# Performance work log

Hardware: AMD Instinct MI355X
Metric: run time of the kernel (lower is better)

Reference implementation:

```python
import jax, jax.numpy as jnp
import numpy as np

N, P, H, K = 8192, 32, 512, 100
D = 2 * P
R = 32  # min(32, max(8, H))


def setup_inputs() -> dict:
    key = jax.random.key(0)
    ks = jax.random.split(key, 12)
    # strictly increasing event times
    dts = jax.random.uniform(ks[0], (N,), dtype=jnp.float32) * 0.1 + 1e-3
    times = jnp.cumsum(dts)
    marks = jax.random.randint(ks[1], (N,), 0, K, dtype=jnp.int32)
    u_inputs = jax.random.normal(ks[2], (N, H), dtype=jnp.float32) * 0.1
    # parameters (match torch init scales)
    lambda_log_real = jax.random.normal(ks[3], (P,), dtype=jnp.float32) * 0.1
    lambda_im = jax.random.normal(ks[4], (P,), dtype=jnp.float32) * 0.05
    V = jnp.eye(D, dtype=jnp.float32) + 0.01 * jax.random.normal(ks[5], (D, D), dtype=jnp.float32)
    B = jax.random.normal(ks[6], (D, H), dtype=jnp.float32) * 0.05
    E = jax.random.normal(ks[7], (D, R), dtype=jnp.float32) * 0.05
    alpha = jax.random.normal(ks[8], (R, K), dtype=jnp.float32) * 0.05
    gate_w = jax.random.normal(ks[9], (P, H), dtype=jnp.float32) * 0.02
    gate_b = jax.random.normal(ks[10], (P,), dtype=jnp.float32) * 0.02
    x0 = jnp.zeros((D,), dtype=jnp.float32)
    return {"times": times, "marks": marks, "u_inputs": u_inputs,
            "lambda_log_real": lambda_log_real, "lambda_im": lambda_im,
            "V": V, "B": B, "E": E, "alpha": alpha,
            "gate_w": gate_w, "gate_b": gate_b, "x0": x0}


def _v_block(V, pr, pi):
    """V @ blockdiag_p([[pr,-pi],[pi,pr]]) for each step n. V:(D,D), pr/pi:(n,P) -> (n,D,D)."""
    Dd = V.shape[0]
    Pp = pr.shape[-1]
    Vr = V.reshape(Dd, Pp, 2)
    col0 = Vr[None, :, :, 0] * pr[:, None, :] + Vr[None, :, :, 1] * pi[:, None, :]
    col1 = -Vr[None, :, :, 0] * pi[:, None, :] + Vr[None, :, :, 1] * pr[:, None, :]
    return jnp.stack([col0, col1], axis=-1).reshape(-1, Dd, Dd)


def reference(times, marks, u_inputs, lambda_log_real, lambda_im, V, B, E, alpha, gate_w, gate_b, x0):
    n = times.shape[0]
    dt = jnp.concatenate([times[:1], jnp.diff(times)])  # (N,) t_0 - 0, t_i - t_{i-1}
    # input-dependent eigenvalues: real = -softplus(log_real) * softplus(Wu+b), imag fixed
    gate = jax.nn.softplus(u_inputs @ gate_w.T + gate_b)           # (N,P)
    real = -jax.nn.softplus(lambda_log_real)[None, :] * gate        # (N,P)
    imag = jnp.broadcast_to(lambda_im[None, :], real.shape)         # (N,P)
    dtc = dt[:, None]
    exps = jnp.exp(real * dtc)
    cosb = jnp.cos(imag * dtc)
    sinb = jnp.sin(imag * dtc)
    a = exps * cosb  # Re(exp(lam dt))
    c = exps * sinb  # Im(exp(lam dt))
    V_inv = jnp.linalg.inv(V)
    # exp(A dt) = V M V^{-1}, M block-rotation per mode
    Aexp = _v_block(V, a, c) @ V_inv                                # (N,D,D)
    # integral (exp(lam dt) - 1)/lam, with dt fallback near lam=0
    denom = real * real + imag * imag
    num_re = a - 1.0
    num_im = c
    qr = (num_re * real + num_im * imag) / (denom + 1e-12)
    qi = (num_im * real - num_re * imag) / (denom + 1e-12)
    small = denom < 1e-8
    qr = jnp.where(small, dtc, qr)
    qi = jnp.where(small, 0.0, qi)
    VMint = _v_block(V, qr, qi)                                     # (N,D,D)
    # cont = V M_int V^{-1} B u  (fuse V^{-1} B u first, avoiding Kmat materialization)
    w = u_inputs @ (V_inv @ B).T                                    # (N,D)
    cont = jnp.einsum('nij,nj->ni', VMint, w)
    cont = jnp.where(dtc > 0, cont, 0.0)
    # mark impulses r_k = E alpha[:, k]
    r = (E @ alpha)[:, marks].T                                     # (N,D)

    def step(x_prev, inp):
        A_i, c_i, r_i = inp
        x_left = A_i @ x_prev + c_i
        x_right = x_left + r_i
        return x_right, (x_right, x_left)

    _, (x_right, x_left) = jax.lax.scan(step, x0, (Aexp, cont, r))
    return x_right, x_left
```

## Files before the change

### kernel.cpp

```cpp
#include <hip/hip_runtime.h>
#include <math.h>

#define NN 8192
#define PP 32
#define HH 512
#define KK 100
#define DD 64
#define RR 32
#define MM 96
#define CH 8
#define GG 1024

#define OFF_VINV   0
#define OFF_M      (OFF_VINV + DD*DD)
#define OFF_EAT    (OFF_M + MM*HH)
#define OFF_RHT    (OFF_EAT + KK*DD)
#define OFF_Y0     (OFF_RHT + KK*DD)
#define OFF_AGG    (OFF_Y0 + DD)
#define OFF_YST    (OFF_AGG + GG*PP*4)
#define OFF_C      (OFF_YST + GG*PP*2)

__device__ __forceinline__ float softplusf(float x) {
    return x > 20.f ? x : log1pf(expf(x));
}

#define IDX(r,c) ((r)*64 + ((c) ^ (((r)&7)<<2)))
__global__ __launch_bounds__(256) void kinv(const float* __restrict__ V,
                                            const float* __restrict__ x0,
                                            float* __restrict__ ws) {
    __shared__ float sm[16384];
    float* Vt = sm;
    float* X  = sm + 4096;
    float* Xt = sm + 8192;
    float* T  = sm + 12288;
    const int t  = threadIdx.x;
    const int i0 = (t >> 4) << 2;
    const int j0 = (t & 15) << 2;

    float nx[4][4];
    #pragma unroll
    for (int r = 0; r < 4; r++) {
        float4 v4 = *(const float4*)&V[(i0 + r) * DD + j0];
        float vv[4] = {v4.x, v4.y, v4.z, v4.w};
        #pragma unroll
        for (int s = 0; s < 4; s++) {
            Vt[IDX(j0 + s, i0 + r)] = vv[s];
            float xv = ((i0 + r) == (j0 + s) ? 2.f : 0.f) - vv[s];
            nx[r][s] = xv;
            X[IDX(i0 + r, j0 + s)] = xv;
            Xt[IDX(j0 + s, i0 + r)] = xv;
        }
    }
    __syncthreads();

    for (int it = 0; it < 3; it++) {
        float acc[4][4];
        #pragma unroll
        for (int r = 0; r < 4; r++)
            #pragma unroll
            for (int s = 0; s < 4; s++) acc[r][s] = 0.f;
        for (int k = 0; k < DD; k++) {
            float4 a = *(float4*)&Vt[IDX(k, i0)];
            float4 bb = *(float4*)&X[IDX(k, j0)];
            float av[4] = {a.x, a.y, a.z, a.w};
            float bv[4] = {bb.x, bb.y, bb.z, bb.w};
            #pragma unroll
            for (int r = 0; r < 4; r++)
                #pragma unroll
                for (int s = 0; s < 4; s++) acc[r][s] = fmaf(av[r], bv[s], acc[r][s]);
        }
        #pragma unroll
        for (int r = 0; r < 4; r++)
            *(float4*)&T[IDX(i0 + r, j0)] = make_float4(acc[r][0], acc[r][1], acc[r][2], acc[r][3]);
        __syncthreads();
        #pragma unroll
        for (int r = 0; r < 4; r++)
            #pragma unroll
            for (int s = 0; s < 4; s++) acc[r][s] = 0.f;
        for (int k = 0; k < DD; k++) {
            float4 a = *(float4*)&Xt[IDX(k, i0)];
            float4 bb = *(float4*)&T[IDX(k, j0)];
            float av[4] = {a.x, a.y, a.z, a.w};
            float bv[4] = {bb.x, bb.y, bb.z, bb.w};
            #pragma unroll
            for (int r = 0; r < 4; r++)
                #pragma unroll
                for (int s = 0; s < 4; s++) acc[r][s] = fmaf(av[r], bv[s], acc[r][s]);
        }
        #pragma unroll
        for (int r = 0; r < 4; r++) {
            float4 xo = *(float4*)&X[IDX(i0 + r, j0)];
            nx[r][0] = 2.f * xo.x - acc[r][0];
            nx[r][1] = 2.f * xo.y - acc[r][1];
            nx[r][2] = 2.f * xo.z - acc[r][2];
            nx[r][3] = 2.f * xo.w - acc[r][3];
        }
        __syncthreads();
        #pragma unroll
        for (int r = 0; r < 4; r++) {
            *(float4*)&X[IDX(i0 + r, j0)] = make_float4(nx[r][0], nx[r][1], nx[r][2], nx[r][3]);
            #pragma unroll
            for (int s = 0; s < 4; s++) Xt[IDX(j0 + s, i0 + r)] = nx[r][s];
        }
        __syncthreads();
    }
    #pragma unroll
    for (int r = 0; r < 4; r++)
        *(float4*)&ws[OFF_VINV + (i0 + r) * DD + j0] =
            make_float4(nx[r][0], nx[r][1], nx[r][2], nx[r][3]);
    float xw[4];
    #pragma unroll
    for (int s = 0; s < 4; s++) xw[s] = x0[j0 + s];
    #pragma unroll
    for (int r = 0; r < 4; r++) {
        float pr = nx[r][0] * xw[0] + nx[r][1] * xw[1] + nx[r][2] * xw[2] + nx[r][3] * xw[3];
        T[(i0 + r) * 17 + (t & 15)] = pr;
    }
    __syncthreads();
    if (t < DD) {
        float s = 0.f;
        #pragma unroll
        for (int jt = 0; jt < 16; jt++) s += T[t * 17 + jt];
        ws[OFF_Y0 + t] = s;
    }
}

__global__ __launch_bounds__(256) void kpre(const float* __restrict__ B,
                                            const float* __restrict__ E,
                                            const float* __restrict__ alpha,
                                            const float* __restrict__ gate_w,
                                            float* __restrict__ ws) {
    int b = blockIdx.x, t = threadIdx.x;
    if (b < 32) {
        int d = b * 2 + (t >> 7);
        int h0 = (t & 127) * 4;
        const float* vr = ws + OFF_VINV + d * DD;
        float4 acc = {0.f, 0.f, 0.f, 0.f};
        for (int j = 0; j < DD; j++) {
            float v = vr[j];
            float4 b4 = *(const float4*)&B[j * HH + h0];
            acc.x = fmaf(v, b4.x, acc.x); acc.y = fmaf(v, b4.y, acc.y);
            acc.z = fmaf(v, b4.z, acc.z); acc.w = fmaf(v, b4.w, acc.w);
        }
        *(float4*)&ws[OFF_M + (32 + d) * HH + h0] = acc;
    } else if (b < 34) {
        #pragma unroll
        for (int s = 0; s < 8; s++) {
            int i4 = (b - 32) * 2048 + t + 256 * s;
            ((float4*)(ws + OFF_M))[i4] = ((const float4*)gate_w)[i4];
        }
    } else {
        __shared__ float vi[DD * 65];
        __shared__ float ea_s[4][DD];
        int kk = (b - 34) * 4 + (t >> 6);
        int d = t & 63;
        for (int idx = t; idx < DD * DD; idx += 256)
            vi[(idx >> 6) * 65 + (idx & 63)] = ws[OFF_VINV + idx];
        float ea = 0.f;
        #pragma unroll
        for (int r = 0; r < RR; r++) ea = fmaf(E[d * RR + r], alpha[r * KK + kk], ea);
        ws[OFF_EAT + kk * DD + d] = ea;
        ea_s[t >> 6][d] = ea;
        __syncthreads();
        float rr = 0.f;
        for (int j = 0; j < DD; j++) rr = fmaf(vi[d * 65 + j], ea_s[t >> 6][j], rr);
        ws[OFF_RHT + kk * DD + d] = rr;
    }
}

__global__ __launch_bounds__(256) void kgemm(const float* __restrict__ u,
                                             float* __restrict__ ws) {
    __shared__ float uT[32 * 64];
    __shared__ float mT[96 * 64];
    int t = threadIdx.x;
    int n0 = blockIdx.x * 32;
    int tn = t & 15, tm = t >> 4;
    const float* Mg = ws + OFF_M;
    float acc[2][6];
    #pragma unroll
    for (int i = 0; i < 2; i++)
        #pragma unroll
        for (int j = 0; j < 6; j++) acc[i][j] = 0.f;

    for (int kc = 0; kc < HH; kc += 64) {
        #pragma unroll
        for (int s = 0; s < 2; s++) {
            int idx = t + 256 * s;
            int r = idx >> 4, c4 = idx & 15;
            float4 f4 = *(const float4*)&u[(n0 + r) * HH + kc + c4 * 4];
            *(float4*)&uT[r * 64 + ((c4 ^ ((r >> 2) & 7)) << 2)] = f4;
        }
        #pragma unroll
        for (int s = 0; s < 6; s++) {
            int idx = t + 256 * s;
            int r = idx >> 4, c4 = idx & 15;
            float4 f4 = *(const float4*)&Mg[r * HH + kc + c4 * 4];
            *(float4*)&mT[r * 64 + ((c4 ^ (r & 7)) << 2)] = f4;
        }
        __syncthreads();
        #pragma unroll
        for (int k4 = 0; k4 < 16; k4++) {
            float4 uu[2], mm[6];
            int swu = (tn >> 1) & 7;
            #pragma unroll
            for (int i = 0; i < 2; i++)
                uu[i] = *(float4*)&uT[(2 * tn + i) * 64 + ((k4 ^ swu) << 2)];
            #pragma unroll
            for (int j = 0; j < 6; j++) {
                int m = 6 * tm + j;
                mm[j] = *(float4*)&mT[m * 64 + ((k4 ^ (m & 7)) << 2)];
            }
            #pragma unroll
            for (int i = 0; i < 2; i++)
                #pragma unroll
                for (int j = 0; j < 6; j++)
                    acc[i][j] += uu[i].x * mm[j].x + uu[i].y * mm[j].y +
                                 uu[i].z * mm[j].z + uu[i].w * mm[j].w;
        }
        __syncthreads();
    }
    #pragma unroll
    for (int i = 0; i < 2; i++)
        #pragma unroll
        for (int j = 0; j < 6; j++)
            ws[OFF_C + (n0 + 2 * tn + i) * MM + 6 * tm + j] = acc[i][j];
}

__device__ __forceinline__ void coef_np(const float* __restrict__ ws,
                                        const int* __restrict__ marks,
                                        int n, int p, float dtv,
                                        float nlr, float imag, float gb,
                                        float& a, float& c, float& br, float& bi) {
    float gate = softplusf(ws[OFF_C + n * MM + p] + gb);
    float real = nlr * gate;
    float e = expf(real * dtv);
    a = e * cosf(imag * dtv);
    c = e * sinf(imag * dtv);
    float denom = real * real + imag * imag;
    float dn = denom + 1e-12f;
    float nre = a - 1.f, nim = c;
    float qr = (nre * real + nim * imag) / dn;
    float qi = (nim * real - nre * imag) / dn;
    if (denom < 1e-8f) { qr = dtv; qi = 0.f; }
    float2 w = *(const float2*)&ws[OFF_C + n * MM + 32 + 2 * p];
    br = qr * w.x - qi * w.y;
    bi = qr * w.y + qi * w.x;
    if (!(dtv > 0.f)) { br = 0.f; bi = 0.f; }
    int mk = marks[n];
    br += ws[OFF_RHT + mk * DD + 2 * p];
    bi += ws[OFF_RHT + mk * DD + 2 * p + 1];
}

__global__ __launch_bounds__(256) void kagg(const float* __restrict__ times,
                                            const int* __restrict__ marks,
                                            const float* __restrict__ llr,
                                            const float* __restrict__ lim,
                                            const float* __restrict__ gate_b,
                                            float* __restrict__ ws) {
    int b = blockIdx.x, t = threadIdx.x;
    int c = t >> 5, p = t & 31;
    int g = b * 8 + c, n0 = g * CH;
    float nlr = -softplusf(llr[p]);
    float imag = lim[p];
    float gb = gate_b[p];
    float zr = 1.f, zi = 0.f, Br = 0.f, Bi = 0.f;
    float tprev = (n0 == 0) ? 0.f : times[n0 - 1];
    for (int i = 0; i < CH; i++) {
        int n = n0 + i;
        float tcur = times[n];
        float dtv = tcur - tprev;
        tprev = tcur;
        float a, cc, br, bi;
        coef_np(ws, marks, n, p, dtv, nlr, imag, gb, a, cc, br, bi);
        float nzr = a * zr - cc * zi;
        float nzi = a * zi + cc * zr;
        float nBr = a * Br - cc * Bi + br;
        float nBi = a * Bi + cc * Br + bi;
        zr = nzr; zi = nzi; Br = nBr; Bi = nBi;
    }
    *(float4*)&ws[OFF_AGG + g * 128 + p * 4] = make_float4(zr, zi, Br, Bi);
}

__device__ __forceinline__ float4 comp_aff(float4 f, float4 g) {
    float4 r;
    r.x = f.x * g.x - f.y * g.y;
    r.y = f.x * g.y + f.y * g.x;
    r.z = f.x * g.z - f.y * g.w + f.z;
    r.w = f.x * g.w + f.y * g.z + f.w;
    return r;
}
__global__ __launch_bounds__(256) void kscan(float* __restrict__ ws) {
    __shared__ float4 sc[256];
    int p = blockIdx.x, t = threadIdx.x;
    float4 ag[4];
    #pragma unroll
    for (int j = 0; j < 4; j++)
        ag[j] = *(float4*)&ws[OFF_AGG + (4 * t + j) * 128 + p * 4];
    float4 val = ag[0];
    val = comp_aff(ag[1], val);
    val = comp_aff(ag[2], val);
    val = comp_aff(ag[3], val);
    sc[t] = val;
    __syncthreads();
    for (int s = 1; s < 256; s <<= 1) {
        float4 o = (t >= s) ? sc[t - s] : make_float4(1.f, 0.f, 0.f, 0.f);
        __syncthreads();
        if (t >= s) val = comp_aff(val, o);
        sc[t] = val;
        __syncthreads();
    }
    float4 Eb = (t > 0) ? sc[t - 1] : make_float4(1.f, 0.f, 0.f, 0.f);
    float2 y0v = *(float2*)&ws[OFF_Y0 + 2 * p];
    float2 ys;
    ys.x = Eb.x * y0v.x - Eb.y * y0v.y + Eb.z;
    ys.y = Eb.x * y0v.y + Eb.y * y0v.x + Eb.w;
    #pragma unroll
    for (int j = 0; j < 4; j++) {
        int g = 4 * t + j;
        *(float2*)&ws[OFF_YST + (g * 32 + p) * 2] = ys;
        float nyr = ag[j].x * ys.x - ag[j].y * ys.y + ag[j].z;
        float nyi = ag[j].x * ys.y + ag[j].y * ys.x + ag[j].w;
        ys.x = nyr; ys.y = nyi;
    }
}

__global__ __launch_bounds__(256) void kout(const float* __restrict__ V,
                                            const float* __restrict__ times,
                                            const int* __restrict__ marks,
                                            const float* __restrict__ llr,
                                            const float* __restrict__ lim,
                                            const float* __restrict__ gate_b,
                                            const float* __restrict__ ws,
                                            float* __restrict__ out) {
    __shared__ float vt[DD * 68];
    __shared__ float yl[DD * 68];
    int b = blockIdx.x, t = threadIdx.x;
    #pragma unroll
    for (int s = 0; s < 16; s++) {
        int idx = t + 256 * s;
        vt[(idx & 63) * 68 + (idx >> 6)] = V[idx];
    }
    int c = t >> 5, p = t & 31;
    int g = b * 8 + c, n0g = g * CH;
    int nb = b * 64;
    float2 y = *(const float2*)&ws[OFF_YST + (g * 32 + p) * 2];
    float nlr = -softplusf(llr[p]);
    float imag = lim[p];
    float gb = gate_b[p];
    float tprev = (n0g == 0) ? 0.f : times[n0g - 1];
    for (int i = 0; i < CH; i++) {
        int n = n0g + i;
        float tcur = times[n];
        float dtv = tcur - tprev;
        tprev = tcur;
        float a, cc, br, bi;
        coef_np(ws, marks, n, p, dtv, nlr, imag, gb, a, cc, br, bi);
        float nyr = a * y.x - cc * y.y + br;
        float nyi = a * y.y + cc * y.x + bi;
        y.x = nyr; y.y = nyi;
        int nl = c * 8 + i;
        *(float2*)&yl[nl * 68 + 2 * p] = y;
    }
    __syncthreads();
    int dt4 = (t & 15) * 4, nt4 = (t >> 4) * 4;
    float acc[4][4];
    #pragma unroll
    for (int r = 0; r < 4; r++)
        #pragma unroll
        for (int s = 0; s < 4; s++) acc[r][s] = 0.f;
    for (int k = 0; k < DD; k++) {
        float4 vv = *(float4*)&vt[k * 68 + dt4];
        float va[4] = {vv.x, vv.y, vv.z, vv.w};
        float yv[4];
        #pragma unroll
        for (int r = 0; r < 4; r++) yv[r] = yl[(nt4 + r) * 68 + k];
        #pragma unroll
        for (int r = 0; r < 4; r++)
            #pragma unroll
            for (int s = 0; s < 4; s++) acc[r][s] = fmaf(yv[r], va[s], acc[r][s]);
    }
    #pragma unroll
    for (int r = 0; r < 4; r++) {
        int n = nb + nt4 + r;
        int mk = marks[n];
        float4 o4 = make_float4(acc[r][0], acc[r][1], acc[r][2], acc[r][3]);
        *(float4*)&out[n * DD + dt4] = o4;
        float4 e4 = *(const float4*)&ws[OFF_EAT + mk * DD + dt4];
        o4.x -= e4.x; o4.y -= e4.y; o4.z -= e4.z; o4.w -= e4.w;
        *(float4*)&out[NN * DD + n * DD + dt4] = o4;
    }
}

extern "C" void kernel_launch(void* const* d_in, const int* in_sizes, int n_in,
                              void* d_out, int out_size, void* d_ws, size_t ws_size,
                              hipStream_t stream) {
    (void)in_sizes; (void)n_in; (void)out_size; (void)ws_size;
    const float* times  = (const float*)d_in[0];
    const int*   marks  = (const int*)d_in[1];
    const float* u      = (const float*)d_in[2];
    const float* llr    = (const float*)d_in[3];
    const float* lim    = (const float*)d_in[4];
    const float* V      = (const float*)d_in[5];
    const float* B      = (const float*)d_in[6];
    const float* E      = (const float*)d_in[7];
    const float* alpha  = (const float*)d_in[8];
    const float* gate_w = (const float*)d_in[9];
    const float* gate_b = (const float*)d_in[10];
    const float* x0     = (const float*)d_in[11];
    float* ws  = (float*)d_ws;
    float* out = (float*)d_out;

    hipLaunchKernelGGL(kinv,  dim3(1),    dim3(256), 0, stream, V, x0, ws);
    hipLaunchKernelGGL(kpre,  dim3(59),   dim3(256), 0, stream, B, E, alpha, gate_w, ws);
    hipLaunchKernelGGL(kgemm, dim3(256),  dim3(256), 0, stream, u, ws);
    hipLaunchKernelGGL(kagg,  dim3(128),  dim3(256), 0, stream, times, marks, llr, lim, gate_b, ws);
    hipLaunchKernelGGL(kscan, dim3(32),   dim3(256), 0, stream, ws);
    hipLaunchKernelGGL(kout,  dim3(128),  dim3(256), 0, stream, V, times, marks, llr, lim, gate_b, ws, out);
}
```

Before: 166.0 us.

## Restructure scan pipeline: finer chunks, cached coefficients, single-block scan, fast math

The pipeline is reorganised. The Newton-Schulz inverse now runs with 512 threads. gate_w is read directly instead of copied into the workspace. The GEMM and aggregation kernels use smaller tiles and more blocks. Per-step coefficients are computed once in the aggregation kernel and stored in the workspace, so the output kernel reuses them instead of recomputing exp, sin and cos. The three-level scan uses 256 block aggregates scanned by one block. Coefficient math switches to fast exp/log, hardware reciprocal and Taylor polynomials for sin and cos, which gives up some accuracy.

Measured after the change: 166.6 us. No clear change (+0.3%).

```diff
diff --git a/kernel.cpp b/kernel.cpp
--- a/kernel.cpp
+++ b/kernel.cpp
@@ -8,24 +8,41 @@
 #define DD 64
 #define RR 32
 #define MM 96
-#define CH 8
-#define GG 1024
+
+#define CH 2
+#define CPB 16
+#define SB 32
+#define NB 256
 
 #define OFF_VINV   0
 #define OFF_M      (OFF_VINV + DD*DD)
-#define OFF_EAT    (OFF_M + MM*HH)
+#define OFF_EAT    (OFF_M + DD*HH)
 #define OFF_RHT    (OFF_EAT + KK*DD)
 #define OFF_Y0     (OFF_RHT + KK*DD)
-#define OFF_AGG    (OFF_Y0 + DD)
-#define OFF_YST    (OFF_AGG + GG*PP*4)
-#define OFF_C      (OFF_YST + GG*PP*2)
-
-__device__ __forceinline__ float softplusf(float x) {
-    return x > 20.f ? x : log1pf(expf(x));
+#define OFF_BAGG   (OFF_Y0 + DD)
+#define OFF_YB     (OFF_BAGG + NB*PP*4)
+#define OFF_C      (OFF_YB + NB*PP*2)
+#define OFF_COEF   (OFF_C + NN*MM)
+
+__device__ __forceinline__ float sp_fast(float x) {
+    return x > 15.f ? x : __logf(1.f + __expf(x));
+}
+__device__ __forceinline__ float rcp_fast(float x) {
+    float r;
+    asm("v_rcp_f32 %0, %1" : "=v"(r) : "v"(x));
+    return r;
+}
+__device__ __forceinline__ float4 comp_aff(float4 f, float4 g) {
+    float4 r;
+    r.x = f.x * g.x - f.y * g.y;
+    r.y = f.x * g.y + f.y * g.x;
+    r.z = f.x * g.z - f.y * g.w + f.z;
+    r.w = f.x * g.w + f.y * g.z + f.w;
+    return r;
 }
 
 #define IDX(r,c) ((r)*64 + ((c) ^ (((r)&7)<<2)))
-__global__ __launch_bounds__(256) void kinv(const float* __restrict__ V,
+__global__ __launch_bounds__(512) void kinv(const float* __restrict__ V,
                                             const float* __restrict__ x0,
                                             float* __restrict__ ws) {
     __shared__ float sm[16384];
@@ -34,12 +51,12 @@
     float* Xt = sm + 8192;
     float* T  = sm + 12288;
     const int t  = threadIdx.x;
-    const int i0 = (t >> 4) << 2;
     const int j0 = (t & 15) << 2;
-
-    float nx[4][4];
-    #pragma unroll
-    for (int r = 0; r < 4; r++) {
+    const int i0 = (t >> 4) << 1;
+
+    float nx[2][4];
+    #pragma unroll
+    for (int r = 0; r < 2; r++) {
         float4 v4 = *(const float4*)&V[(i0 + r) * DD + j0];
         float vv[4] = {v4.x, v4.y, v4.z, v4.w};
         #pragma unroll
@@ -47,48 +64,48 @@
             Vt[IDX(j0 + s, i0 + r)] = vv[s];
             float xv = ((i0 + r) == (j0 + s) ? 2.f : 0.f) - vv[s];
             nx[r][s] = xv;
-            X[IDX(i0 + r, j0 + s)] = xv;
             Xt[IDX(j0 + s, i0 + r)] = xv;
         }
+        *(float4*)&X[IDX(i0 + r, j0)] = make_float4(nx[r][0], nx[r][1], nx[r][2], nx[r][3]);
     }
     __syncthreads();
 
     for (int it = 0; it < 3; it++) {
-        float acc[4][4];
-        #pragma unroll
-        for (int r = 0; r < 4; r++)
+        float acc[2][4];
+        #pragma unroll
+        for (int r = 0; r < 2; r++)
             #pragma unroll
             for (int s = 0; s < 4; s++) acc[r][s] = 0.f;
         for (int k = 0; k < DD; k++) {
-            float4 a = *(float4*)&Vt[IDX(k, i0)];
-            float4 bb = *(float4*)&X[IDX(k, j0)];
-            float av[4] = {a.x, a.y, a.z, a.w};
-            float bv[4] = {bb.x, bb.y, bb.z, bb.w};
-            #pragma unroll
-            for (int r = 0; r < 4; r++)
-                #pragma unroll
-                for (int s = 0; s < 4; s++) acc[r][s] = fmaf(av[r], bv[s], acc[r][s]);
-        }
-        #pragma unroll
-        for (int r = 0; r < 4; r++)
+            float2 a2 = *(float2*)&Vt[IDX(k, i0)];
+            float4 b4 = *(float4*)&X[IDX(k, j0)];
+            float bv[4] = {b4.x, b4.y, b4.z, b4.w};
+            #pragma unroll
+            for (int s = 0; s < 4; s++) {
+                acc[0][s] = fmaf(a2.x, bv[s], acc[0][s]);
+                acc[1][s] = fmaf(a2.y, bv[s], acc[1][s]);
+            }
+        }
+        #pragma unroll
+        for (int r = 0; r < 2; r++)
             *(float4*)&T[IDX(i0 + r, j0)] = make_float4(acc[r][0], acc[r][1], acc[r][2], acc[r][3]);
         __syncthreads();
         #pragma unroll
-        for (int r = 0; r < 4; r++)
+        for (int r = 0; r < 2; r++)
             #pragma unroll
             for (int s = 0; s < 4; s++) acc[r][s] = 0.f;
         for (int k = 0; k < DD; k++) {
-            float4 a = *(float4*)&Xt[IDX(k, i0)];
-            float4 bb = *(float4*)&T[IDX(k, j0)];
-            float av[4] = {a.x, a.y, a.z, a.w};
-            float bv[4] = {bb.x, bb.y, bb.z, bb.w};
-            #pragma unroll
-            for (int r = 0; r < 4; r++)
-                #pragma unroll
-                for (int s = 0; s < 4; s++) acc[r][s] = fmaf(av[r], bv[s], acc[r][s]);
-        }
-        #pragma unroll
-        for (int r = 0; r < 4; r++) {
+            float2 a2 = *(float2*)&Xt[IDX(k, i0)];
+            float4 b4 = *(float4*)&T[IDX(k, j0)];
+            float bv[4] = {b4.x, b4.y, b4.z, b4.w};
+            #pragma unroll
+            for (int s = 0; s < 4; s++) {
+                acc[0][s] = fmaf(a2.x, bv[s], acc[0][s]);
+                acc[1][s] = fmaf(a2.y, bv[s], acc[1][s]);
+            }
+        }
+        #pragma unroll
+        for (int r = 0; r < 2; r++) {
             float4 xo = *(float4*)&X[IDX(i0 + r, j0)];
             nx[r][0] = 2.f * xo.x - acc[r][0];
             nx[r][1] = 2.f * xo.y - acc[r][1];
@@ -97,7 +114,7 @@
         }
         __syncthreads();
         #pragma unroll
-        for (int r = 0; r < 4; r++) {
+        for (int r = 0; r < 2; r++) {
             *(float4*)&X[IDX(i0 + r, j0)] = make_float4(nx[r][0], nx[r][1], nx[r][2], nx[r][3]);
             #pragma unroll
             for (int s = 0; s < 4; s++) Xt[IDX(j0 + s, i0 + r)] = nx[r][s];
@@ -105,14 +122,13 @@
         __syncthreads();
     }
     #pragma unroll
-    for (int r = 0; r < 4; r++)
+    for (int r = 0; r < 2; r++)
         *(float4*)&ws[OFF_VINV + (i0 + r) * DD + j0] =
             make_float4(nx[r][0], nx[r][1], nx[r][2], nx[r][3]);
-    float xw[4];
-    #pragma unroll
-    for (int s = 0; s < 4; s++) xw[s] = x0[j0 + s];
-    #pragma unroll
-    for (int r = 0; r < 4; r++) {
+    float4 xq = *(const float4*)&x0[j0];
+    float xw[4] = {xq.x, xq.y, xq.z, xq.w};
+    #pragma unroll
+    for (int r = 0; r < 2; r++) {
         float pr = nx[r][0] * xw[0] + nx[r][1] * xw[1] + nx[r][2] * xw[2] + nx[r][3] * xw[3];
         T[(i0 + r) * 17 + (t & 15)] = pr;
     }
@@ -128,7 +144,6 @@
 __global__ __launch_bounds__(256) void kpre(const float* __restrict__ B,
                                             const float* __restrict__ E,
                                             const float* __restrict__ alpha,
-                                            const float* __restrict__ gate_w,
                                             float* __restrict__ ws) {
     int b = blockIdx.x, t = threadIdx.x;
     if (b < 32) {
@@ -142,17 +157,11 @@
             acc.x = fmaf(v, b4.x, acc.x); acc.y = fmaf(v, b4.y, acc.y);
             acc.z = fmaf(v, b4.z, acc.z); acc.w = fmaf(v, b4.w, acc.w);
         }
-        *(float4*)&ws[OFF_M + (32 + d) * HH + h0] = acc;
-    } else if (b < 34) {
-        #pragma unroll
-        for (int s = 0; s < 8; s++) {
-            int i4 = (b - 32) * 2048 + t + 256 * s;
-            ((float4*)(ws + OFF_M))[i4] = ((const float4*)gate_w)[i4];
-        }
+        *(float4*)&ws[OFF_M + d * HH + h0] = acc;
     } else {
         __shared__ float vi[DD * 65];
         __shared__ float ea_s[4][DD];
-        int kk = (b - 34) * 4 + (t >> 6);
+        int kk = (b - 32) * 4 + (t >> 6);
         int d = t & 63;
         for (int idx = t; idx < DD * DD; idx += 256)
             vi[(idx >> 6) * 65 + (idx & 63)] = ws[OFF_VINV + idx];
@@ -168,52 +177,52 @@
     }
 }
 
-__global__ __launch_bounds__(256) void kgemm(const float* __restrict__ u,
-                                             float* __restrict__ ws) {
-    __shared__ float uT[32 * 64];
+__global__ __launch_bounds__(256, 2) void kgemm(const float* __restrict__ u,
+                                                const float* __restrict__ gate_w,
+                                                float* __restrict__ ws) {
+    __shared__ float uT[16 * 64];
     __shared__ float mT[96 * 64];
     int t = threadIdx.x;
-    int n0 = blockIdx.x * 32;
-    int tn = t & 15, tm = t >> 4;
-    const float* Mg = ws + OFF_M;
-    float acc[2][6];
+    int n0 = blockIdx.x * 16;
+    int tn = t & 7, tm = t >> 3;
+    float acc[2][3];
     #pragma unroll
     for (int i = 0; i < 2; i++)
         #pragma unroll
-        for (int j = 0; j < 6; j++) acc[i][j] = 0.f;
+        for (int j = 0; j < 3; j++) acc[i][j] = 0.f;
 
     for (int kc = 0; kc < HH; kc += 64) {
-        #pragma unroll
-        for (int s = 0; s < 2; s++) {
-            int idx = t + 256 * s;
-            int r = idx >> 4, c4 = idx & 15;
+        {
+            int r = t >> 4, c4 = t & 15;
             float4 f4 = *(const float4*)&u[(n0 + r) * HH + kc + c4 * 4];
-            *(float4*)&uT[r * 64 + ((c4 ^ ((r >> 2) & 7)) << 2)] = f4;
+            *(float4*)&uT[r * 64 + ((c4 ^ (r & 7)) << 2)] = f4;
         }
         #pragma unroll
         for (int s = 0; s < 6; s++) {
             int idx = t + 256 * s;
             int r = idx >> 4, c4 = idx & 15;
-            float4 f4 = *(const float4*)&Mg[r * HH + kc + c4 * 4];
+            const float* src = (r < 32) ? &gate_w[r * HH] : &ws[OFF_M + (r - 32) * HH];
+            float4 f4 = *(const float4*)&src[kc + c4 * 4];
             *(float4*)&mT[r * 64 + ((c4 ^ (r & 7)) << 2)] = f4;
         }
         __syncthreads();
         #pragma unroll
         for (int k4 = 0; k4 < 16; k4++) {
-            float4 uu[2], mm[6];
-            int swu = (tn >> 1) & 7;
-            #pragma unroll
-            for (int i = 0; i < 2; i++)
-                uu[i] = *(float4*)&uT[(2 * tn + i) * 64 + ((k4 ^ swu) << 2)];
-            #pragma unroll
-            for (int j = 0; j < 6; j++) {
-                int m = 6 * tm + j;
+            float4 uu[2], mm[3];
+            #pragma unroll
+            for (int i = 0; i < 2; i++) {
+                int rr = 2 * tn + i;
+                uu[i] = *(float4*)&uT[rr * 64 + ((k4 ^ (rr & 7)) << 2)];
+            }
+            #pragma unroll
+            for (int j = 0; j < 3; j++) {
+                int m = 3 * tm + j;
                 mm[j] = *(float4*)&mT[m * 64 + ((k4 ^ (m & 7)) << 2)];
             }
             #pragma unroll
             for (int i = 0; i < 2; i++)
                 #pragma unroll
-                for (int j = 0; j < 6; j++)
+                for (int j = 0; j < 3; j++)
                     acc[i][j] += uu[i].x * mm[j].x + uu[i].y * mm[j].y +
                                  uu[i].z * mm[j].z + uu[i].w * mm[j].w;
         }
@@ -222,173 +231,159 @@
     #pragma unroll
     for (int i = 0; i < 2; i++)
         #pragma unroll
-        for (int j = 0; j < 6; j++)
-            ws[OFF_C + (n0 + 2 * tn + i) * MM + 6 * tm + j] = acc[i][j];
-}
-
-__device__ __forceinline__ void coef_np(const float* __restrict__ ws,
-                                        const int* __restrict__ marks,
-                                        int n, int p, float dtv,
-                                        float nlr, float imag, float gb,
-                                        float& a, float& c, float& br, float& bi) {
-    float gate = softplusf(ws[OFF_C + n * MM + p] + gb);
+        for (int j = 0; j < 3; j++)
+            ws[OFF_C + (n0 + 2 * tn + i) * MM + 3 * tm + j] = acc[i][j];
+}
+
+__device__ __forceinline__ float4 coef_fast(const float* __restrict__ ws,
+                                            const int* __restrict__ marks,
+                                            int n, int p, float dtv,
+                                            float nlr, float imag, float gb) {
+    float gate = sp_fast(ws[OFF_C + n * MM + p] + gb);
     float real = nlr * gate;
-    float e = expf(real * dtv);
-    a = e * cosf(imag * dtv);
-    c = e * sinf(imag * dtv);
+    float e = __expf(real * dtv);
+    float x = imag * dtv, x2 = x * x;
+    float cb = 1.f - x2 * (0.5f - x2 * (1.f / 24.f));
+    float sb = x * (1.f - x2 * ((1.f / 6.f) - x2 * (1.f / 120.f)));
+    float a = e * cb, c = e * sb;
     float denom = real * real + imag * imag;
-    float dn = denom + 1e-12f;
+    float inv = rcp_fast(denom + 1e-12f);
     float nre = a - 1.f, nim = c;
-    float qr = (nre * real + nim * imag) / dn;
-    float qi = (nim * real - nre * imag) / dn;
+    float qr = (nre * real + nim * imag) * inv;
+    float qi = (nim * real - nre * imag) * inv;
     if (denom < 1e-8f) { qr = dtv; qi = 0.f; }
     float2 w = *(const float2*)&ws[OFF_C + n * MM + 32 + 2 * p];
-    br = qr * w.x - qi * w.y;
-    bi = qr * w.y + qi * w.x;
+    float br = qr * w.x - qi * w.y;
+    float bi = qr * w.y + qi * w.x;
     if (!(dtv > 0.f)) { br = 0.f; bi = 0.f; }
     int mk = marks[n];
-    br += ws[OFF_RHT + mk * DD + 2 * p];
-    bi += ws[OFF_RHT + mk * DD + 2 * p + 1];
-}
-
-__global__ __launch_bounds__(256) void kagg(const float* __restrict__ times,
-                                            const int* __restrict__ marks,
-                                            const float* __restrict__ llr,
-                                            const float* __restrict__ lim,
-                                            const float* __restrict__ gate_b,
-                                            float* __restrict__ ws) {
+    float2 rh = *(const float2*)&ws[OFF_RHT + mk * DD + 2 * p];
+    return make_float4(a, c, br + rh.x, bi + rh.y);
+}
+
+__global__ __launch_bounds__(512, 2) void kagg(const float* __restrict__ times,
+                                               const int* __restrict__ marks,
+                                               const float* __restrict__ llr,
+                                               const float* __restrict__ lim,
+                                               const float* __restrict__ gate_b,
+                                               float* __restrict__ ws) {
+    __shared__ float4 smagg[CPB][PP];
     int b = blockIdx.x, t = threadIdx.x;
     int c = t >> 5, p = t & 31;
-    int g = b * 8 + c, n0 = g * CH;
-    float nlr = -softplusf(llr[p]);
-    float imag = lim[p];
-    float gb = gate_b[p];
-    float zr = 1.f, zi = 0.f, Br = 0.f, Bi = 0.f;
+    int n0 = b * SB + c * CH;
+    float nlr = -sp_fast(llr[p]);
+    float imag = lim[p], gb = gate_b[p];
     float tprev = (n0 == 0) ? 0.f : times[n0 - 1];
+    float4* coef = (float4*)(ws + OFF_COEF);
+    float4 agg = make_float4(1.f, 0.f, 0.f, 0.f);
+    #pragma unroll
     for (int i = 0; i < CH; i++) {
         int n = n0 + i;
         float tcur = times[n];
-        float dtv = tcur - tprev;
-        tprev = tcur;
-        float a, cc, br, bi;
-        coef_np(ws, marks, n, p, dtv, nlr, imag, gb, a, cc, br, bi);
-        float nzr = a * zr - cc * zi;
-        float nzi = a * zi + cc * zr;
-        float nBr = a * Br - cc * Bi + br;
-        float nBi = a * Bi + cc * Br + bi;
-        zr = nzr; zi = nzi; Br = nBr; Bi = nBi;
-    }
-    *(float4*)&ws[OFF_AGG + g * 128 + p * 4] = make_float4(zr, zi, Br, Bi);
-}
-
-__device__ __forceinline__ float4 comp_aff(float4 f, float4 g) {
-    float4 r;
-    r.x = f.x * g.x - f.y * g.y;
-    r.y = f.x * g.y + f.y * g.x;
-    r.z = f.x * g.z - f.y * g.w + f.z;
-    r.w = f.x * g.w + f.y * g.z + f.w;
-    return r;
-}
+        float dtv = tcur - tprev; tprev = tcur;
+        float4 cf = coef_fast(ws, marks, n, p, dtv, nlr, imag, gb);
+        coef[n * PP + p] = cf;
+        agg = comp_aff(cf, agg);
+    }
+    smagg[c][p] = agg;
+    __syncthreads();
+    if (t < PP) {
+        float4 T = make_float4(1.f, 0.f, 0.f, 0.f);
+        #pragma unroll
+        for (int cc = 0; cc < CPB; cc++) T = comp_aff(smagg[cc][t], T);
+        *(float4*)&ws[OFF_BAGG + (b * PP + t) * 4] = T;
+    }
+}
+
 __global__ __launch_bounds__(256) void kscan(float* __restrict__ ws) {
-    __shared__ float4 sc[256];
-    int p = blockIdx.x, t = threadIdx.x;
-    float4 ag[4];
-    #pragma unroll
-    for (int j = 0; j < 4; j++)
-        ag[j] = *(float4*)&ws[OFF_AGG + (4 * t + j) * 128 + p * 4];
-    float4 val = ag[0];
-    val = comp_aff(ag[1], val);
-    val = comp_aff(ag[2], val);
-    val = comp_aff(ag[3], val);
-    sc[t] = val;
-    __syncthreads();
-    for (int s = 1; s < 256; s <<= 1) {
-        float4 o = (t >= s) ? sc[t - s] : make_float4(1.f, 0.f, 0.f, 0.f);
-        __syncthreads();
-        if (t >= s) val = comp_aff(val, o);
-        sc[t] = val;
-        __syncthreads();
-    }
-    float4 Eb = (t > 0) ? sc[t - 1] : make_float4(1.f, 0.f, 0.f, 0.f);
-    float2 y0v = *(float2*)&ws[OFF_Y0 + 2 * p];
-    float2 ys;
-    ys.x = Eb.x * y0v.x - Eb.y * y0v.y + Eb.z;
-    ys.y = Eb.x * y0v.y + Eb.y * y0v.x + Eb.w;
-    #pragma unroll
-    for (int j = 0; j < 4; j++) {
-        int g = 4 * t + j;
-        *(float2*)&ws[OFF_YST + (g * 32 + p) * 2] = ys;
-        float nyr = ag[j].x * ys.x - ag[j].y * ys.y + ag[j].z;
-        float nyi = ag[j].x * ys.y + ag[j].y * ys.x + ag[j].w;
-        ys.x = nyr; ys.y = nyi;
-    }
-}
-
-__global__ __launch_bounds__(256) void kout(const float* __restrict__ V,
-                                            const float* __restrict__ times,
-                                            const int* __restrict__ marks,
-                                            const float* __restrict__ llr,
-                                            const float* __restrict__ lim,
-                                            const float* __restrict__ gate_b,
-                                            const float* __restrict__ ws,
-                                            float* __restrict__ out) {
+    __shared__ float4 sseg[8][PP];
+    __shared__ float4 qseg[8][PP];
+    int t = threadIdx.x;
+    int p = t & 31, s = t >> 5;
+    const float4* bagg = (const float4*)(ws + OFF_BAGG);
+    float4 S = make_float4(1.f, 0.f, 0.f, 0.f);
+    for (int b = 32 * s; b < 32 * s + 32; b++) S = comp_aff(bagg[b * PP + p], S);
+    sseg[s][p] = S;
+    __syncthreads();
+    if (t < PP) {
+        float4 Q = make_float4(1.f, 0.f, 0.f, 0.f);
+        #pragma unroll
+        for (int ss = 0; ss < 8; ss++) { qseg[ss][t] = Q; Q = comp_aff(sseg[ss][t], Q); }
+    }
+    __syncthreads();
+    float2 y0v = *(const float2*)&ws[OFF_Y0 + 2 * p];
+    float4 Q = qseg[s][p];
+    float2 y;
+    y.x = Q.x * y0v.x - Q.y * y0v.y + Q.z;
+    y.y = Q.x * y0v.y + Q.y * y0v.x + Q.w;
+    for (int b = 32 * s; b < 32 * s + 32; b++) {
+        *(float2*)&ws[OFF_YB + (b * PP + p) * 2] = y;
+        float4 A = bagg[b * PP + p];
+        float nyr = A.x * y.x - A.y * y.y + A.z;
+        float nyi = A.x * y.y + A.y * y.x + A.w;
+        y.x = nyr; y.y = nyi;
+    }
+}
+
+__global__ __launch_bounds__(512, 2) void kout(const float* __restrict__ V,
+                                               const int* __restrict__ marks,
+                                               const float* __restrict__ ws,
+                                               float* __restrict__ out) {
     __shared__ float vt[DD * 68];
-    __shared__ float yl[DD * 68];
+    __shared__ float yl[SB * 68];
+    __shared__ float4 smagg[CPB][PP];
     int b = blockIdx.x, t = threadIdx.x;
     #pragma unroll
-    for (int s = 0; s < 16; s++) {
-        int idx = t + 256 * s;
+    for (int s = 0; s < 8; s++) {
+        int idx = t + 512 * s;
         vt[(idx & 63) * 68 + (idx >> 6)] = V[idx];
     }
     int c = t >> 5, p = t & 31;
-    int g = b * 8 + c, n0g = g * CH;
-    int nb = b * 64;
-    float2 y = *(const float2*)&ws[OFF_YST + (g * 32 + p) * 2];
-    float nlr = -softplusf(llr[p]);
-    float imag = lim[p];
-    float gb = gate_b[p];
-    float tprev = (n0g == 0) ? 0.f : times[n0g - 1];
-    for (int i = 0; i < CH; i++) {
-        int n = n0g + i;
-        float tcur = times[n];
-        float dtv = tcur - tprev;
-        tprev = tcur;
-        float a, cc, br, bi;
-        coef_np(ws, marks, n, p, dtv, nlr, imag, gb, a, cc, br, bi);
-        float nyr = a * y.x - cc * y.y + br;
-        float nyi = a * y.y + cc * y.x + bi;
+    int n0 = b * SB + c * CH;
+    const float4* coef = (const float4*)(ws + OFF_COEF);
+    float4 cf0 = coef[(n0 + 0) * PP + p];
+    float4 cf1 = coef[(n0 + 1) * PP + p];
+    smagg[c][p] = comp_aff(cf1, cf0);
+    __syncthreads();
+    float2 y = *(const float2*)&ws[OFF_YB + (b * PP + p) * 2];
+    #pragma unroll
+    for (int cc = 0; cc < CPB - 1; cc++) {
+        float4 A = smagg[cc][p];
+        if (cc < c) {
+            float nyr = A.x * y.x - A.y * y.y + A.z;
+            float nyi = A.x * y.y + A.y * y.x + A.w;
+            y.x = nyr; y.y = nyi;
+        }
+    }
+    {
+        float nyr = cf0.x * y.x - cf0.y * y.y + cf0.z;
+        float nyi = cf0.x * y.y + cf0.y * y.x + cf0.w;
         y.x = nyr; y.y = nyi;
-        int nl = c * 8 + i;
-        *(float2*)&yl[nl * 68 + 2 * p] = y;
-    }
-    __syncthreads();
-    int dt4 = (t & 15) * 4, nt4 = (t >> 4) * 4;
-    float acc[4][4];
-    #pragma unroll
-    for (int r = 0; r < 4; r++)
-        #pragma unroll
-        for (int s = 0; s < 4; s++) acc[r][s] = 0.f;
+        *(float2*)&yl[(c * CH + 0) * 68 + 2 * p] = y;
+        nyr = cf1.x * y.x - cf1.y * y.y + cf1.z;
+        nyi = cf1.x * y.y + cf1.y * y.x + cf1.w;
+        y.x = nyr; y.y = nyi;
+        *(float2*)&yl[(c * CH + 1) * 68 + 2 * p] = y;
+    }
+    __syncthreads();
+    int dt4 = (t & 15) * 4;
+    int nr = t >> 4;
+    float acc[4] = {0.f, 0.f, 0.f, 0.f};
     for (int k = 0; k < DD; k++) {
         float4 vv = *(float4*)&vt[k * 68 + dt4];
-        float va[4] = {vv.x, vv.y, vv.z, vv.w};
-        float yv[4];
-        #pragma unroll
-        for (int r = 0; r < 4; r++) yv[r] = yl[(nt4 + r) * 68 + k];
-        #pragma unroll
-        for (int r = 0; r < 4; r++)
-            #pragma unroll
-            for (int s = 0; s < 4; s++) acc[r][s] = fmaf(yv[r], va[s], acc[r][s]);
-    }
-    #pragma unroll
-    for (int r = 0; r < 4; r++) {
-        int n = nb + nt4 + r;
-        int mk = marks[n];
-        float4 o4 = make_float4(acc[r][0], acc[r][1], acc[r][2], acc[r][3]);
-        *(float4*)&out[n * DD + dt4] = o4;
-        float4 e4 = *(const float4*)&ws[OFF_EAT + mk * DD + dt4];
-        o4.x -= e4.x; o4.y -= e4.y; o4.z -= e4.z; o4.w -= e4.w;
-        *(float4*)&out[NN * DD + n * DD + dt4] = o4;
-    }
+        float yv = yl[nr * 68 + k];
+        acc[0] = fmaf(yv, vv.x, acc[0]);
+        acc[1] = fmaf(yv, vv.y, acc[1]);
+        acc[2] = fmaf(yv, vv.z, acc[2]);
+        acc[3] = fmaf(yv, vv.w, acc[3]);
+    }
+    int n = b * SB + nr;
+    int mk = marks[n];
+    float4 o4 = make_float4(acc[0], acc[1], acc[2], acc[3]);
+    *(float4*)&out[n * DD + dt4] = o4;
+    float4 e4 = *(const float4*)&ws[OFF_EAT + mk * DD + dt4];
+    o4.x -= e4.x; o4.y -= e4.y; o4.z -= e4.z; o4.w -= e4.w;
+    *(float4*)&out[NN * DD + n * DD + dt4] = o4;
 }
 
 extern "C" void kernel_launch(void* const* d_in, const int* in_sizes, int n_in,
@@ -410,10 +405,10 @@
     float* ws  = (float*)d_ws;
     float* out = (float*)d_out;
 
-    hipLaunchKernelGGL(kinv,  dim3(1),    dim3(256), 0, stream, V, x0, ws);
-    hipLaunchKernelGGL(kpre,  dim3(59),   dim3(256), 0, stream, B, E, alpha, gate_w, ws);
-    hipLaunchKernelGGL(kgemm, dim3(256),  dim3(256), 0, stream, u, ws);
-    hipLaunchKernelGGL(kagg,  dim3(128),  dim3(256), 0, stream, times, marks, llr, lim, gate_b, ws);
-    hipLaunchKernelGGL(kscan, dim3(32),   dim3(256), 0, stream, ws);
-    hipLaunchKernelGGL(kout,  dim3(128),  dim3(256), 0, stream, V, times, marks, llr, lim, gate_b, ws, out);
-}
+    hipLaunchKernelGGL(kinv,  dim3(1),   dim3(512), 0, stream, V, x0, ws);
+    hipLaunchKernelGGL(kpre,  dim3(57),  dim3(256), 0, stream, B, E, alpha, ws);
+    hipLaunchKernelGGL(kgemm, dim3(512), dim3(256), 0, stream, u, gate_w, ws);
+    hipLaunchKernelGGL(kagg,  dim3(256), dim3(512), 0, stream, times, marks, llr, lim, gate_b, ws);
+    hipLaunchKernelGGL(kscan, dim3(1),   dim3(256), 0, stream, ws);
+    hipLaunchKernelGGL(kout,  dim3(256), dim3(512), 0, stream, V, marks, ws, out);
+}
```
